# Performance work log

Measured on AMD Instinct MI355X. Metric: run time of the kernel, lower is better.

Reference implementation:

```python
import jax, jax.numpy as jnp
import numpy as np

E = 8          # num_experts
K = 2          # top_k
CAPF = 1.25    # capacity_factor


def setup_inputs() -> dict:
    key = jax.random.key(0)
    ks = jax.random.split(key, 6)
    B, T, C = 4, 2048, 1024
    x = jax.random.normal(ks[0], (B, T, C), jnp.float32)
    noise = jax.random.normal(ks[1], (B, T, E), jnp.float32)  # stands in for torch.randn_like
    Wr = jax.random.normal(ks[2], (C, E), jnp.float32) * 0.02   # topkroute_linear
    Wn = jax.random.normal(ks[3], (C, E), jnp.float32) * 0.02   # noise_linear
    W1 = jax.random.normal(ks[4], (E, C, 4 * C), jnp.float32) * 0.02  # expert up-proj
    W2 = jax.random.normal(ks[5], (E, 4 * C, C), jnp.float32) * 0.02  # expert down-proj
    return {"x": x, "noise": noise, "Wr": Wr, "Wn": Wn, "W1": W1, "W2": W2}


def reference(x, noise, Wr, Wn, W1, W2):
    B, T, C = x.shape
    N = B * T
    cap = int(N * K / E * CAPF)  # expert_capacity (static)

    # --- NoisyTopkRouter ---
    logits = x @ Wr                                  # [B,T,E]
    noise_logits = x @ Wn                            # [B,T,E]
    noisy = logits + noise * jax.nn.softplus(noise_logits)
    _, idx = jax.lax.top_k(noisy, K)                 # [B,T,K]
    mask_bte = (idx[..., None] == jnp.arange(E)).any(axis=-2)       # [B,T,E]
    gating = jax.nn.softmax(jnp.where(mask_bte, noisy, -jnp.inf), axis=-1)

    flat_x = x.reshape(N, C)
    flat_g = gating.reshape(N, E)

    # --- capacity-limited dispatch (token order, first `cap` per expert) ---
    mask = mask_bte.reshape(N, E).T                  # [E,N]
    rank = jnp.cumsum(mask, axis=1) - 1              # position within expert
    keep = mask & (rank < cap)
    slot = jnp.where(keep, rank, cap)                # overflow -> dump slot `cap`
    tok = jnp.where(keep, jnp.arange(N)[None, :], N) # dropped -> pad token `N`
    s2t = jnp.full((E, cap + 1), N, dtype=jnp.int32)
    s2t = s2t.at[jnp.arange(E)[:, None], slot].set(tok.astype(jnp.int32))[:, :cap]  # [E,cap]

    # --- gather, grouped GEMM (Linear-SiLU-Linear), weight, scatter-add ---
    x_pad = jnp.concatenate([flat_x, jnp.zeros((1, C), flat_x.dtype)], axis=0)
    xin = x_pad[s2t]                                 # [E,cap,C]
    h = jax.nn.silu(jnp.einsum('enc,ech->enh', xin, W1))
    out = jnp.einsum('enh,ehc->enc', h, W2)          # [E,cap,C]
    g_pad = jnp.concatenate([flat_g, jnp.zeros((1, E), flat_g.dtype)], axis=0)
    gate = g_pad[s2t, jnp.arange(E)[:, None]]        # [E,cap]
    weighted = out * gate[..., None]
    upd = jnp.zeros((N + 1, C), x.dtype).at[s2t.reshape(-1)].add(weighted.reshape(-1, C))
    return upd[:N].reshape(B, T, C)
```

## Files before the change

kernel.cpp:

```cpp
#include <hip/hip_runtime.h>
#include <hip/hip_bf16.h>
#include <math.h>

#define C_DIM 1024
#define H_DIM 4096
#define E_NUM 8

typedef __bf16 bf16x8 __attribute__((ext_vector_type(8)));
typedef float f32x4 __attribute__((ext_vector_type(4)));

__device__ __forceinline__ unsigned short f2bf(float f) {
  union { float f; unsigned u; } v; v.f = f;
  unsigned r = v.u + 0x7FFFu + ((v.u >> 16) & 1u);
  return (unsigned short)(r >> 16);
}

__device__ __forceinline__ void gload16(const short* g, short* l) {
  __builtin_amdgcn_global_load_lds(
      (const __attribute__((address_space(1))) unsigned int*)g,
      (__attribute__((address_space(3))) unsigned int*)l, 16, 0, 0);
}

__global__ __launch_bounds__(256) void router_kernel(
    const float* __restrict__ x, const float* __restrict__ noise,
    const float* __restrict__ Wr, const float* __restrict__ Wn,
    int2* __restrict__ idx_out, float2* __restrict__ gate_out, int N)
{
  int t = blockIdx.x;
  int tid = threadIdx.x;
  const float* xrow = x + (size_t)t * C_DIM;
  float accR[E_NUM], accN[E_NUM];
#pragma unroll
  for (int e = 0; e < E_NUM; e++) { accR[e] = 0.f; accN[e] = 0.f; }
  for (int c = tid; c < C_DIM; c += 256) {
    float xv = xrow[c];
    const float* wr = Wr + (size_t)c * E_NUM;
    const float* wn = Wn + (size_t)c * E_NUM;
#pragma unroll
    for (int e = 0; e < E_NUM; e++) {
      accR[e] = fmaf(xv, wr[e], accR[e]);
      accN[e] = fmaf(xv, wn[e], accN[e]);
    }
  }
#pragma unroll
  for (int e = 0; e < E_NUM; e++) {
    for (int off = 32; off > 0; off >>= 1) {
      accR[e] += __shfl_down(accR[e], off, 64);
      accN[e] += __shfl_down(accN[e], off, 64);
    }
  }
  __shared__ float red[4][2 * E_NUM];
  int lane = tid & 63, wave = tid >> 6;
  if (lane == 0) {
#pragma unroll
    for (int e = 0; e < E_NUM; e++) { red[wave][e] = accR[e]; red[wave][E_NUM + e] = accN[e]; }
  }
  __syncthreads();
  if (tid == 0) {
    float ns[E_NUM];
#pragma unroll
    for (int e = 0; e < E_NUM; e++) {
      float lg = red[0][e] + red[1][e] + red[2][e] + red[3][e];
      float nl = red[0][E_NUM + e] + red[1][E_NUM + e] + red[2][E_NUM + e] + red[3][E_NUM + e];
      float sp = fmaxf(nl, 0.f) + log1pf(expf(-fabsf(nl)));
      ns[e] = lg + noise[(size_t)t * E_NUM + e] * sp;
    }
    int i1 = 0; float m1 = ns[0];
    int i2 = -1; float m2 = -INFINITY;
#pragma unroll
    for (int e = 1; e < E_NUM; e++) {
      float v = ns[e];
      if (v > m1) { m2 = m1; i2 = i1; m1 = v; i1 = e; }
      else if (v > m2) { m2 = v; i2 = e; }
    }
    float e2 = expf(m2 - m1);
    float s = 1.f + e2;
    gate_out[t] = make_float2(1.f / s, e2 / s);
    idx_out[t] = make_int2(i1, i2);
  }
}

__global__ __launch_bounds__(256) void scan_kernel(
    const int2* __restrict__ idx, const float2* __restrict__ gates,
    int* __restrict__ s2t, float* __restrict__ gslot, int* __restrict__ counts,
    int N, int cap)
{
  int e = blockIdx.x;
  int tid = threadIdx.x;
  for (int s = tid; s < cap; s += 256) { s2t[(size_t)e * cap + s] = N; gslot[(size_t)e * cap + s] = 0.f; }
  __syncthreads();
  __shared__ int wtot[4];
  int lane = tid & 63, wave = tid >> 6;
  int running = 0;
  for (int base = 0; base < N; base += 256) {
    int t = base + tid;
    int2 ix = idx[t];
    bool flag = (ix.x == e) || (ix.y == e);
    unsigned long long m = __ballot(flag);
    int rank = __popcll(m & ((1ull << lane) - 1ull));
    if (lane == 0) wtot[wave] = __popcll(m);
    __syncthreads();
    int woff = 0;
    for (int w = 0; w < wave; w++) woff += wtot[w];
    int slot = running + woff + rank;
    if (flag && slot < cap) {
      s2t[(size_t)e * cap + slot] = t;
      gslot[(size_t)e * cap + slot] = (ix.x == e) ? gates[t].x : gates[t].y;
    }
    running += wtot[0] + wtot[1] + wtot[2] + wtot[3];
    __syncthreads();
  }
  if (tid == 0) counts[e] = min(running, cap);
}

__global__ __launch_bounds__(256) void convert_x_kernel(
    const float* __restrict__ src, short* __restrict__ dst, int n8)
{
  int i = blockIdx.x * 256 + threadIdx.x;
  if (i >= n8) return;
  const float4* s = (const float4*)src + (size_t)i * 2;
  float4 a = s[0], b = s[1];
  union { unsigned short us[8]; uint4 v; } o;
  o.us[0] = f2bf(a.x); o.us[1] = f2bf(a.y); o.us[2] = f2bf(a.z); o.us[3] = f2bf(a.w);
  o.us[4] = f2bf(b.x); o.us[5] = f2bf(b.y); o.us[6] = f2bf(b.z); o.us[7] = f2bf(b.w);
  ((uint4*)dst)[i] = o.v;
}

__global__ __launch_bounds__(256) void transpose_convert_kernel(
    const float* __restrict__ src, short* __restrict__ dst,
    int R, int Cc)
{
  src += (size_t)blockIdx.z * R * Cc;
  dst += (size_t)blockIdx.z * (size_t)R * Cc;
  __shared__ float tile[64][65];
  int c0 = blockIdx.x * 64, r0 = blockIdx.y * 64;
  int tid = threadIdx.x;
  int tr = tid >> 4, tc = (tid & 15) * 4;
#pragma unroll
  for (int p = 0; p < 4; p++) {
    int r = p * 16 + tr;
    float4 v = *(const float4*)(src + (size_t)(r0 + r) * Cc + c0 + tc);
    tile[r][tc] = v.x; tile[r][tc + 1] = v.y; tile[r][tc + 2] = v.z; tile[r][tc + 3] = v.w;
  }
  __syncthreads();
#pragma unroll
  for (int p = 0; p < 4; p++) {
    int c = p * 16 + tr;
    union { unsigned short us[4]; ushort4 v; } o;
#pragma unroll
    for (int j = 0; j < 4; j++) o.us[j] = f2bf(tile[tc + j][c]);
    *(ushort4*)(dst + (size_t)(c0 + c) * R + r0 + tc) = o.v;
  }
}

template<int MODE>
__global__ __launch_bounds__(256, 2) void gemm_moe(
    const short* __restrict__ Abase, const short* __restrict__ Wt,
    const int* __restrict__ s2t, const float* __restrict__ gslot,
    const int* __restrict__ counts, void* __restrict__ outp,
    int cap, int N)
{
  __shared__ short As[2][8192];
  __shared__ short Bs[2][8192];

  int e = blockIdx.z;
  int cnt = counts[e];
  int row0 = blockIdx.y * 128;
  if (row0 >= cnt) return;
  int col0 = blockIdx.x * 128;

  int tid = threadIdx.x;
  int w = tid >> 6, l = tid & 63;
  int wr = w >> 1, wc = w & 1;
  int rowT = tid & 127, kbT = tid >> 7;

  constexpr int KS = (MODE == 0) ? C_DIM : H_DIM;
  constexpr int NS = KS / 64;

  const short *pA, *pB;
  if (MODE == 0) {
    int tok = min(s2t[e * cap + row0 + rowT], N - 1);
    pA = Abase + (size_t)tok * C_DIM;
    pB = Wt + (size_t)e * (C_DIM * H_DIM) + (size_t)(col0 + rowT) * C_DIM;
  } else {
    pA = Abase + ((size_t)e * cap + row0 + rowT) * H_DIM;
    pB = Wt + (size_t)e * (C_DIM * H_DIM) + (size_t)(col0 + rowT) * H_DIM;
  }

  int aBase = (l >> 4) * 1024 + (wr * 64 + (l & 15)) * 8;
  int bBase = (l >> 4) * 1024 + (wc * 64 + (l & 15)) * 8;

  f32x4 acc[4][4];
#pragma unroll
  for (int m = 0; m < 4; m++)
#pragma unroll
    for (int n = 0; n < 4; n++) acc[m][n] = 0.f;

#define STAGE(k0, buf) { \
  _Pragma("unroll") for (int j = 0; j < 4; ++j) { \
    int kb = kbT + 2 * j; \
    gload16(pA + (k0) + kb * 8, &As[buf][kb * 1024 + rowT * 8]); \
    gload16(pB + (k0) + kb * 8, &Bs[buf][kb * 1024 + rowT * 8]); \
  } }

  STAGE(0, 0);
  int cur = 0;
#pragma unroll 1
  for (int i = 0; i < NS; ++i) {
    __syncthreads();
    bf16x8 af[4][2], bg[4][2];
#pragma unroll
    for (int m = 0; m < 4; m++)
#pragma unroll
      for (int kk = 0; kk < 2; kk++)
        af[m][kk] = *(const bf16x8*)&As[cur][aBase + m * 128 + kk * 4096];
#pragma unroll
    for (int n = 0; n < 4; n++)
#pragma unroll
      for (int kk = 0; kk < 2; kk++)
        bg[n][kk] = *(const bf16x8*)&Bs[cur][bBase + n * 128 + kk * 4096];
    if (i + 1 < NS) STAGE((i + 1) * 64, cur ^ 1);
#pragma unroll
    for (int m = 0; m < 4; m++)
#pragma unroll
      for (int n = 0; n < 4; n++) {
        acc[m][n] = __builtin_amdgcn_mfma_f32_16x16x32_bf16(af[m][0], bg[n][0], acc[m][n], 0, 0, 0);
        acc[m][n] = __builtin_amdgcn_mfma_f32_16x16x32_bf16(af[m][1], bg[n][1], acc[m][n], 0, 0, 0);
      }
    cur ^= 1;
  }
#undef STAGE

  int orow = row0 + wr * 64 + (l >> 4) * 4;
  int ocol = col0 + wc * 64 + (l & 15);
  if (MODE == 0) {
    short* hE = (short*)outp + (size_t)e * cap * H_DIM;
#pragma unroll
    for (int m = 0; m < 4; m++)
#pragma unroll
      for (int r = 0; r < 4; r++) {
        size_t rb = (size_t)(orow + m * 16 + r) * H_DIM + ocol;
#pragma unroll
        for (int n = 0; n < 4; n++) {
          float v = acc[m][n][r];
          hE[rb + n * 16] = (short)f2bf(v / (1.f + expf(-v)));
        }
      }
  } else {
    float* out = (float*)outp;
#pragma unroll
    for (int m = 0; m < 4; m++)
#pragma unroll
      for (int r = 0; r < 4; r++) {
        int slot = row0 + wr * 64 + m * 16 + (l >> 4) * 4 + r;
        int tok = s2t[e * cap + slot];
        if (tok < N) {
          float g = gslot[e * cap + slot];
          float* op = out + (size_t)tok * C_DIM + ocol;
#pragma unroll
          for (int n = 0; n < 4; n++)
            atomicAdd(op + n * 16, g * acc[m][n][r]);
        }
      }
  }
}

extern "C" void kernel_launch(void* const* d_in, const int* in_sizes, int n_in,
                              void* d_out, int out_size, void* d_ws, size_t ws_size,
                              hipStream_t stream)
{
  const float* x     = (const float*)d_in[0];
  const float* noise = (const float*)d_in[1];
  const float* Wr    = (const float*)d_in[2];
  const float* Wn    = (const float*)d_in[3];
  const float* W1    = (const float*)d_in[4];
  const float* W2    = (const float*)d_in[5];
  float* out = (float*)d_out;

  int N = in_sizes[0] / C_DIM;
  int cap = (int)((double)N * 2.0 / E_NUM * 1.25);
  int rows = cap / 128;

  size_t off = 0;
  auto alloc = [&](size_t bytes) -> char* {
    char* r = (char*)d_ws + off;
    off += (bytes + 255) & ~(size_t)255;
    return r;
  };
  int2*   idx    = (int2*)alloc((size_t)N * sizeof(int2));
  float2* gates  = (float2*)alloc((size_t)N * sizeof(float2));
  int*    s2t    = (int*)alloc((size_t)E_NUM * cap * sizeof(int));
  float*  gslot  = (float*)alloc((size_t)E_NUM * cap * sizeof(float));
  int*    counts = (int*)alloc(E_NUM * sizeof(int));
  short*  xbf    = (short*)alloc((size_t)N * C_DIM * sizeof(short));
  short*  W1t    = (short*)alloc((size_t)E_NUM * C_DIM * H_DIM * sizeof(short));
  short*  W2t    = (short*)alloc((size_t)E_NUM * C_DIM * H_DIM * sizeof(short));
  short*  h      = (short*)alloc((size_t)E_NUM * cap * H_DIM * sizeof(short));
  (void)ws_size;

  hipMemsetAsync(d_out, 0, (size_t)out_size * sizeof(float), stream);
  router_kernel<<<N, 256, 0, stream>>>(x, noise, Wr, Wn, idx, gates, N);
  scan_kernel<<<E_NUM, 256, 0, stream>>>(idx, gates, s2t, gslot, counts, N, cap);
  convert_x_kernel<<<(N * C_DIM / 8 + 255) / 256, 256, 0, stream>>>(x, xbf, N * C_DIM / 8);
  transpose_convert_kernel<<<dim3(H_DIM / 64, C_DIM / 64, E_NUM), 256, 0, stream>>>(
      W1, W1t, C_DIM, H_DIM);
  transpose_convert_kernel<<<dim3(C_DIM / 64, H_DIM / 64, E_NUM), 256, 0, stream>>>(
      W2, W2t, H_DIM, C_DIM);

  gemm_moe<0><<<dim3(H_DIM / 128, rows, E_NUM), 256, 0, stream>>>(
      xbf, W1t, s2t, gslot, counts, h, cap, N);
  gemm_moe<1><<<dim3(C_DIM / 128, rows, E_NUM), 256, 0, stream>>>(
      h, W2t, s2t, gslot, counts, out, cap, N);
}
```

Before: 936.8 us.

## Split-K the down-projection, remap grid for expert interleaving, fold gate into SiLU output

```diff
diff --git a/kernel.cpp b/kernel.cpp
--- a/kernel.cpp
+++ b/kernel.cpp
@@ -158,33 +158,42 @@
     const short* __restrict__ Abase, const short* __restrict__ Wt,
     const int* __restrict__ s2t, const float* __restrict__ gslot,
     const int* __restrict__ counts, void* __restrict__ outp,
-    int cap, int N)
+    int cap, int N, int rows)
 {
   __shared__ short As[2][8192];
   __shared__ short Bs[2][8192];
 
-  int e = blockIdx.z;
+  int flat = blockIdx.x;
+  int e = flat & 7;
+  int s = flat >> 3;
+  int perGrp = rows * 8;
+  int grp = s / perGrp;
+  int loc = s - grp * perGrp;
+  int r = loc >> 3;
+  int c, kc;
+  if (MODE == 0) { c = grp * 8 + (loc & 7); kc = 0; }
+  else           { c = loc & 7;             kc = grp; }
+
   int cnt = counts[e];
-  int row0 = blockIdx.y * 128;
+  int row0 = r * 128;
   if (row0 >= cnt) return;
-  int col0 = blockIdx.x * 128;
+  int col0 = c * 128;
 
   int tid = threadIdx.x;
   int w = tid >> 6, l = tid & 63;
   int wr = w >> 1, wc = w & 1;
   int rowT = tid & 127, kbT = tid >> 7;
 
-  constexpr int KS = (MODE == 0) ? C_DIM : H_DIM;
-  constexpr int NS = KS / 64;
+  const int NS = 16;
 
   const short *pA, *pB;
   if (MODE == 0) {
-    int tok = min(s2t[e * cap + row0 + rowT], N - 1);
+    int tok = min(s2t[(size_t)e * cap + row0 + rowT], N - 1);
     pA = Abase + (size_t)tok * C_DIM;
     pB = Wt + (size_t)e * (C_DIM * H_DIM) + (size_t)(col0 + rowT) * C_DIM;
   } else {
-    pA = Abase + ((size_t)e * cap + row0 + rowT) * H_DIM;
-    pB = Wt + (size_t)e * (C_DIM * H_DIM) + (size_t)(col0 + rowT) * H_DIM;
+    pA = Abase + ((size_t)e * cap + row0 + rowT) * H_DIM + kc * 1024;
+    pB = Wt + (size_t)e * (C_DIM * H_DIM) + (size_t)(col0 + rowT) * H_DIM + kc * 1024;
   }
 
   int aBase = (l >> 4) * 1024 + (wr * 64 + (l & 15)) * 8;
@@ -238,12 +247,14 @@
 #pragma unroll
     for (int m = 0; m < 4; m++)
 #pragma unroll
-      for (int r = 0; r < 4; r++) {
-        size_t rb = (size_t)(orow + m * 16 + r) * H_DIM + ocol;
+      for (int rr = 0; rr < 4; rr++) {
+        int slot = orow + m * 16 + rr;
+        float g = gslot[(size_t)e * cap + slot];
+        size_t rb = (size_t)slot * H_DIM + ocol;
 #pragma unroll
         for (int n = 0; n < 4; n++) {
-          float v = acc[m][n][r];
-          hE[rb + n * 16] = (short)f2bf(v / (1.f + expf(-v)));
+          float v = acc[m][n][rr];
+          hE[rb + n * 16] = (short)f2bf(g * (v / (1.f + expf(-v))));
         }
       }
   } else {
@@ -251,15 +262,14 @@
 #pragma unroll
     for (int m = 0; m < 4; m++)
 #pragma unroll
-      for (int r = 0; r < 4; r++) {
-        int slot = row0 + wr * 64 + m * 16 + (l >> 4) * 4 + r;
-        int tok = s2t[e * cap + slot];
+      for (int rr = 0; rr < 4; rr++) {
+        int slot = orow + m * 16 + rr;
+        int tok = s2t[(size_t)e * cap + slot];
         if (tok < N) {
-          float g = gslot[e * cap + slot];
           float* op = out + (size_t)tok * C_DIM + ocol;
 #pragma unroll
           for (int n = 0; n < 4; n++)
-            atomicAdd(op + n * 16, g * acc[m][n][r]);
+            atomicAdd(op + n * 16, acc[m][n][rr]);
         }
       }
   }
@@ -307,8 +317,8 @@
   transpose_convert_kernel<<<dim3(C_DIM / 64, H_DIM / 64, E_NUM), 256, 0, stream>>>(
       W2, W2t, H_DIM, C_DIM);
 
-  gemm_moe<0><<<dim3(H_DIM / 128, rows, E_NUM), 256, 0, stream>>>(
-      xbf, W1t, s2t, gslot, counts, h, cap, N);
-  gemm_moe<1><<<dim3(C_DIM / 128, rows, E_NUM), 256, 0, stream>>>(
-      h, W2t, s2t, gslot, counts, out, cap, N);
-}
+  gemm_moe<0><<<dim3(E_NUM * (H_DIM / 128 / 8) * (rows * 8)), 256, 0, stream>>>(
+      xbf, W1t, s2t, gslot, counts, h, cap, N, rows);
+  gemm_moe<1><<<dim3(E_NUM * 4 * (rows * 8)), 256, 0, stream>>>(
+      h, W2t, s2t, gslot, counts, out, cap, N, rows);
+}
```

Measured after the change: 941.0 us. No clear change (+0.4%).
